# Kernel optimization log

Measured on AMD Instinct MI355X. Metric: run time of the kernel, lower is better.

Reference implementation:

```python
import jax, jax.numpy as jnp
import numpy as np

N_NODES = 100000  # size_u + size_v + size_w
N_MP = 3          # metapaths vv, uu, ww
N_EDGES = 1000000
D_IN = 64
D_OUT = 64


def setup_inputs() -> dict:
    key = jax.random.key(0)
    k1, k2, k3, k4 = jax.random.split(key, 4)
    x = jax.random.normal(k1, (N_NODES, D_IN), dtype=jnp.float32)
    # per-metapath GCNConv weight (glorot-ish scale)
    W = jax.random.normal(k2, (N_MP, D_IN, D_OUT), dtype=jnp.float32) * (1.0 / np.sqrt(D_IN))
    edge_index = jax.random.randint(k3, (N_MP, 2, N_EDGES), 0, N_NODES, dtype=jnp.int64)
    edge_weight = jax.random.uniform(k4, (N_MP, N_EDGES), dtype=jnp.float32)
    return {"x": x, "W": W, "edge_index": edge_index, "edge_weight": edge_weight}


def _gcn_conv(x, w_mat, row, col, ew, num_nodes):
    # gcn_norm without self-loops: deg[i] = sum of edge weights into i
    deg = jax.ops.segment_sum(ew, col, num_segments=num_nodes)
    dinv = jnp.where(deg > 0, jax.lax.rsqrt(jnp.where(deg > 0, deg, 1.0)), 0.0)
    norm = dinv[row] * ew * dinv[col]          # [E]
    h = x @ w_mat                               # [N, D_OUT]
    msg = h[row] * norm[:, None]                # [E, D_OUT] gather + scale
    return jax.ops.segment_sum(msg, col, num_segments=num_nodes)  # scatter-add


def reference(x, W, edge_index, edge_weight):
    num_nodes = x.shape[0]
    outs = []
    for i in range(N_MP):  # small fixed loop over structurally distinct encoders
        row = edge_index[i, 0]
        col = edge_index[i, 1]
        out = _gcn_conv(x, W[i], row, col, edge_weight[i], num_nodes)
        outs.append(jax.nn.relu(out))  # act=nn.ReLU
    return jnp.stack(outs)  # [3, N, D_OUT]; dropout omitted (eval mode)
```

## Files before the change

kernel.cpp:

```cpp
#include <hip/hip_runtime.h>
#include <hip/hip_fp16.h>

#define NNODES 100000
#define NMP 3
#define NEDGES 1000000
#define D 64
#define NTOT (NMP * NNODES)
#define BINW 1024
#define NBIN 293
#define CAPB 10944
#define T1 5632
#define RPT 11
#define OVCAP 131072

typedef __attribute__((ext_vector_type(8))) short bf16x8;
typedef __attribute__((ext_vector_type(4))) float floatx4;

__device__ __forceinline__ unsigned short f2bf(float f) {
    unsigned u = __float_as_uint(f);
    u = (u + 0x7FFFu + ((u >> 16) & 1u)) >> 16;
    return (unsigned short)u;
}
__device__ __forceinline__ __half2 u2h(unsigned u) {
    __half2 r;
    *reinterpret_cast<unsigned*>(&r) = u;
    return r;
}

__global__ __launch_bounds__(512) void split_kernel(const int* __restrict__ ei,
                                                    const float* __restrict__ ew,
                                                    int* __restrict__ gcur,
                                                    int* __restrict__ ovcur,
                                                    int* __restrict__ ovf,
                                                    uint2* __restrict__ A) {
    __shared__ uint2 stage[T1];
    __shared__ unsigned short sbin[T1];
    __shared__ int hist[NBIN], lbase[NBIN], gbase[NBIN], lcur[NBIN];
    __shared__ int sh[512];
    const int t = threadIdx.x;
    const int mp = blockIdx.y;
    const int e0 = blockIdx.x * T1;
    const int nrec = min(T1, NEDGES - e0);
    for (int i = t; i < NBIN; i += 512) hist[i] = 0;
    __syncthreads();
    unsigned key[RPT]; float w[RPT]; int bn[RPT];
#pragma unroll
    for (int i = 0; i < RPT; ++i) {
        int e = e0 + i * 512 + t;
        bn[i] = -1;
        if (e < NEDGES) {
            int r = ei[(mp * 2 + 0) * NEDGES + e];
            int c = ei[(mp * 2 + 1) * NEDGES + e];
            w[i] = ew[mp * NEDGES + e];
            int cflat = mp * NNODES + c;
            int rflat = mp * NNODES + r;
            int b = cflat >> 10;
            bn[i] = b;
            key[i] = ((unsigned)(cflat & 1023) << 19) | (unsigned)rflat;
            atomicAdd(&hist[b], 1);
        }
    }
    __syncthreads();
    int v = (t < NBIN) ? hist[t] : 0;
    sh[t] = v;
    __syncthreads();
    for (int d = 1; d < 512; d <<= 1) {
        int add = (t >= d) ? sh[t - d] : 0;
        __syncthreads();
        sh[t] += add;
        __syncthreads();
    }
    if (t < NBIN) {
        int ex = sh[t] - v;
        lbase[t] = ex;
        lcur[t] = ex;
        gbase[t] = v ? atomicAdd(&gcur[t], v) : 0;
    }
    __syncthreads();
#pragma unroll
    for (int i = 0; i < RPT; ++i) {
        if (bn[i] >= 0) {
            int s = atomicAdd(&lcur[bn[i]], 1);
            stage[s] = make_uint2(key[i], __float_as_uint(w[i]));
            sbin[s] = (unsigned short)bn[i];
        }
    }
    __syncthreads();
    for (int s = t; s < nrec; s += 512) {
        int b = sbin[s];
        uint2 rec = stage[s];
        int pos = gbase[b] + (s - lbase[b]);
        if (pos < CAPB) {
            A[(size_t)b * CAPB + pos] = rec;
        } else {
            int op = atomicAdd(ovcur, 1);
            if (op < OVCAP) {
                int cflat = (b << 10) | (int)(rec.x >> 19);
                ovf[3 * op] = cflat;
                ovf[3 * op + 1] = (int)(rec.x & 0x7FFFFu);
                ovf[3 * op + 2] = (int)rec.y;
            }
        }
    }
}

__global__ __launch_bounds__(256) void compact2_kernel(const int* __restrict__ gcur,
                                                       const uint2* __restrict__ A,
                                                       const int* __restrict__ ovcur,
                                                       const int* __restrict__ ovf,
                                                       uint2* __restrict__ C,
                                                       int2* __restrict__ nodeoff,
                                                       float* __restrict__ dinv) {
    const int bin = blockIdx.x;
    __shared__ int cnt[BINW];
    __shared__ float wsum[BINW];
    __shared__ int pos[BINW];
    __shared__ int sh[256];
    const int t = threadIdx.x;
    for (int i = t; i < BINW; i += 256) { cnt[i] = 0; wsum[i] = 0.0f; }
    __syncthreads();
    const int len = min(gcur[bin], CAPB);
    const uint2* Ab = A + (size_t)bin * CAPB;
    for (int p = t; p < len; p += 256) {
        uint2 rec = Ab[p];
        atomicAdd(&cnt[rec.x >> 19], 1);
        atomicAdd(&wsum[rec.x >> 19], __uint_as_float(rec.y));
    }
    const int ovn = min(*ovcur, OVCAP);
    for (int i = t; i < ovn; i += 256) {
        int cflat = ovf[3 * i];
        if ((cflat >> 10) == bin) {
            atomicAdd(&cnt[cflat & 1023], 1);
            atomicAdd(&wsum[cflat & 1023], __int_as_float(ovf[3 * i + 2]));
        }
    }
    __syncthreads();
    int c0 = cnt[4 * t], c1 = cnt[4 * t + 1], c2 = cnt[4 * t + 2], c3 = cnt[4 * t + 3];
    int vsum = c0 + c1 + c2 + c3;
    sh[t] = vsum;
    __syncthreads();
    for (int d = 1; d < 256; d <<= 1) {
        int add = (t >= d) ? sh[t - d] : 0;
        __syncthreads();
        sh[t] += add;
        __syncthreads();
    }
    const int base = bin * CAPB;
    const int lim = base + CAPB;
    int p0 = base + sh[t] - vsum;
    int p1 = p0 + c0, p2 = p1 + c1, p3 = p2 + c2;
    pos[4 * t] = p0; pos[4 * t + 1] = p1; pos[4 * t + 2] = p2; pos[4 * t + 3] = p3;
    int starts[4] = {p0, p1, p2, p3};
    int cs[4] = {c0, c1, c2, c3};
#pragma unroll
    for (int j = 0; j < 4; ++j) {
        int cl = 4 * t + j;
        int node = (bin << 10) + cl;
        if (node < NTOT) {
            nodeoff[node] = make_int2(starts[j], cs[j]);
            float dg = wsum[cl];
            dinv[node] = (dg > 0.0f) ? rsqrtf(dg) : 0.0f;
        }
    }
    __syncthreads();
    for (int p = t; p < len; p += 256) {
        uint2 rec = Ab[p];
        int s = atomicAdd(&pos[rec.x >> 19], 1);
        if (s < lim) C[s] = make_uint2(rec.x & 0x7FFFFu, rec.y);
    }
    for (int i = t; i < ovn; i += 256) {
        int cflat = ovf[3 * i];
        if ((cflat >> 10) == bin) {
            int s = atomicAdd(&pos[cflat & 1023], 1);
            if (s < lim) C[s] = make_uint2((unsigned)ovf[3 * i + 1], (unsigned)ovf[3 * i + 2]);
        }
    }
}

__global__ __launch_bounds__(256) void prep_w_kernel(const float* __restrict__ W,
                                                     unsigned short* __restrict__ wT) {
    int idx = blockIdx.x * 256 + threadIdx.x;
    if (idx >= NMP * D * D) return;
    int mp = idx >> 12, rem = idx & 4095;
    int k = rem >> 6, n = rem & 63;
    wT[(mp * D + n) * D + k] = f2bf(W[idx]);
}

__global__ __launch_bounds__(256) void gemm_kernel(const float* __restrict__ x,
                                                   const unsigned short* __restrict__ wT,
                                                   const float* __restrict__ dinv,
                                                   unsigned short* __restrict__ h) {
    const int wave = threadIdx.x >> 6;
    const int lane = threadIdx.x & 63;
    const int rowbase = (blockIdx.x * 4 + wave) * 16;
    if (rowbase >= NNODES) return;
    const int m = lane & 15;
    const int q = lane >> 4;
    const float4* xr = (const float4*)(x + (size_t)(rowbase + m) * D);
    bf16x8 a[2];
#pragma unroll
    for (int kc = 0; kc < 2; ++kc) {
        float4 x0 = xr[kc * 8 + q * 2];
        float4 x1 = xr[kc * 8 + q * 2 + 1];
        a[kc][0] = f2bf(x0.x); a[kc][1] = f2bf(x0.y);
        a[kc][2] = f2bf(x0.z); a[kc][3] = f2bf(x0.w);
        a[kc][4] = f2bf(x1.x); a[kc][5] = f2bf(x1.y);
        a[kc][6] = f2bf(x1.z); a[kc][7] = f2bf(x1.w);
    }
#pragma unroll
    for (int mp = 0; mp < NMP; ++mp) {
        float dv = dinv[mp * NNODES + rowbase + m];
#pragma unroll
        for (int nt = 0; nt < 4; ++nt) {
            const bf16x8* bp = (const bf16x8*)(wT + (size_t)(mp * D + nt * 16 + m) * D);
            bf16x8 b0 = bp[q];
            bf16x8 b1 = bp[4 + q];
            floatx4 acc = {0.f, 0.f, 0.f, 0.f};
            acc = __builtin_amdgcn_mfma_f32_16x16x32_bf16(b0, a[0], acc, 0, 0, 0);
            acc = __builtin_amdgcn_mfma_f32_16x16x32_bf16(b1, a[1], acc, 0, 0, 0);
            unsigned v0 = (unsigned)__half_as_ushort(__float2half(acc[0] * dv)) |
                          ((unsigned)__half_as_ushort(__float2half(acc[1] * dv)) << 16);
            unsigned v1 = (unsigned)__half_as_ushort(__float2half(acc[2] * dv)) |
                          ((unsigned)__half_as_ushort(__float2half(acc[3] * dv)) << 16);
            *(uint2*)(h + ((size_t)mp * NNODES + rowbase + m) * D + nt * 16 + q * 4) =
                make_uint2(v0, v1);
        }
    }
}

__global__ __launch_bounds__(256) void gather_kernel(const int2* __restrict__ nodeoff,
                                                     const uint2* __restrict__ dense,
                                                     const unsigned short* __restrict__ h,
                                                     const float* __restrict__ dinv,
                                                     float* __restrict__ out) {
    const int tid = threadIdx.x;
    const int wave = tid >> 6, lane = tid & 63;
    const int sub = lane >> 5;
    const int g = (lane >> 3) & 3;
    const int f = lane & 7;
    const int w = blockIdx.x * 8 + wave * 2 + sub;
    int2 off = nodeoff[w];
    const int start = off.x, end = off.x + off.y;
    const uint4* hp = (const uint4*)h;
    __half2 acc2[4];
    acc2[0] = __float2half2_rn(0.0f); acc2[1] = __float2half2_rn(0.0f);
    acc2[2] = __float2half2_rn(0.0f); acc2[3] = __float2half2_rn(0.0f);
    if (end > start) {
        const int last = end - 1;
        uint2 prA = dense[min(start + g, last)];
        uint2 prB = dense[min(start + 4 + g, last)];
        uint4 hvA = hp[(size_t)prA.x * 8 + f];
        for (int p = start; p < end; p += 4) {
            uint2 prC = dense[min(p + 8 + g, last)];
            uint4 hvB = hp[(size_t)prB.x * 8 + f];
            float wgt = (p + g < end) ? __uint_as_float(prA.y) : 0.0f;
            __half2 wp = __float2half2_rn(wgt);
            acc2[0] = __hfma2(u2h(hvA.x), wp, acc2[0]);
            acc2[1] = __hfma2(u2h(hvA.y), wp, acc2[1]);
            acc2[2] = __hfma2(u2h(hvA.z), wp, acc2[2]);
            acc2[3] = __hfma2(u2h(hvA.w), wp, acc2[3]);
            prA = prB; hvA = hvB; prB = prC;
        }
    }
    float acc[8];
    acc[0] = __low2float(acc2[0]); acc[1] = __high2float(acc2[0]);
    acc[2] = __low2float(acc2[1]); acc[3] = __high2float(acc2[1]);
    acc[4] = __low2float(acc2[2]); acc[5] = __high2float(acc2[2]);
    acc[6] = __low2float(acc2[3]); acc[7] = __high2float(acc2[3]);
#pragma unroll
    for (int j = 0; j < 8; ++j) {
        acc[j] += __shfl_xor(acc[j], 8);
        acc[j] += __shfl_xor(acc[j], 16);
    }
    float dv = dinv[w];
    if (g < 2) {
        float4 o = g ? make_float4(acc[4], acc[5], acc[6], acc[7])
                     : make_float4(acc[0], acc[1], acc[2], acc[3]);
        o.x = fmaxf(o.x * dv, 0.0f);
        o.y = fmaxf(o.y * dv, 0.0f);
        o.z = fmaxf(o.z * dv, 0.0f);
        o.w = fmaxf(o.w * dv, 0.0f);
        ((float4*)out)[(size_t)w * 16 + f * 2 + g] = o;
    }
}

extern "C" void kernel_launch(void* const* d_in, const int* in_sizes, int n_in,
                              void* d_out, int out_size, void* d_ws, size_t ws_size,
                              hipStream_t stream) {
    const float* x  = (const float*)d_in[0];
    const float* W  = (const float*)d_in[1];
    const int*   ei = (const int*)d_in[2];
    const float* ew = (const float*)d_in[3];
    float* out = (float*)d_out;

    char* ws = (char*)d_ws;
    uint2* A           = (uint2*)(ws + 0);
    unsigned short* h  = (unsigned short*)(ws + 0);
    uint2* C           = (uint2*)(ws + 38400000);
    int2*  nodeoff     = (int2*)(ws + 64052736);
    float* dinv        = (float*)(ws + 66452736);
    unsigned short* wT = (unsigned short*)(ws + 67652736);
    int*   gcur        = (int*)(ws + 67677312);
    int*   ovcur       = (int*)(ws + 67678484);
    int*   ovf         = (int*)(ws + 67678488);

    hipMemsetAsync(gcur, 0, 1176, stream);

    split_kernel<<<dim3((NEDGES + T1 - 1) / T1, NMP), 512, 0, stream>>>(ei, ew, gcur,
                                                                        ovcur, ovf, A);
    compact2_kernel<<<NBIN, 256, 0, stream>>>(gcur, A, ovcur, ovf, C, nodeoff, dinv);
    prep_w_kernel<<<(NMP * D * D + 255) / 256, 256, 0, stream>>>(W, wT);
    gemm_kernel<<<(NNODES / 16 + 3) / 4, 256, 0, stream>>>(x, wT, dinv, h);
    gather_kernel<<<NTOT / 8, 256, 0, stream>>>(nodeoff, C, h, dinv, out);
}
```

Measured before the change: 285.6 us.

## Use wave-shuffle block scans, widen compact blocks, one node per wave in gather

```diff
diff --git a/kernel.cpp b/kernel.cpp
--- a/kernel.cpp
+++ b/kernel.cpp
@@ -27,6 +27,31 @@
     return r;
 }
 
+__device__ __forceinline__ int block_excl_scan(int v, int t, int nthreads, int* wsums) {
+    const int lane = t & 63, wv = t >> 6;
+    int s = v;
+#pragma unroll
+    for (int d = 1; d < 64; d <<= 1) {
+        int u = __shfl_up(s, d);
+        if (lane >= d) s += u;
+    }
+    if (lane == 63) wsums[wv] = s;
+    __syncthreads();
+    if (wv == 0) {
+        const int nw = nthreads >> 6;
+        int ws = (lane < nw) ? wsums[lane] : 0;
+#pragma unroll
+        for (int d = 1; d < 8; d <<= 1) {
+            int u = __shfl_up(ws, d);
+            if (lane >= d) ws += u;
+        }
+        if (lane < nw) wsums[lane] = ws;
+    }
+    __syncthreads();
+    int wbase = wv ? wsums[wv - 1] : 0;
+    return wbase + s - v;
+}
+
 __global__ __launch_bounds__(512) void split_kernel(const int* __restrict__ ei,
                                                     const float* __restrict__ ew,
                                                     int* __restrict__ gcur,
@@ -36,7 +61,7 @@
     __shared__ uint2 stage[T1];
     __shared__ unsigned short sbin[T1];
     __shared__ int hist[NBIN], lbase[NBIN], gbase[NBIN], lcur[NBIN];
-    __shared__ int sh[512];
+    __shared__ int wsums[8];
     const int t = threadIdx.x;
     const int mp = blockIdx.y;
     const int e0 = blockIdx.x * T1;
@@ -62,16 +87,8 @@
     }
     __syncthreads();
     int v = (t < NBIN) ? hist[t] : 0;
-    sh[t] = v;
-    __syncthreads();
-    for (int d = 1; d < 512; d <<= 1) {
-        int add = (t >= d) ? sh[t - d] : 0;
-        __syncthreads();
-        sh[t] += add;
-        __syncthreads();
-    }
+    int ex = block_excl_scan(v, t, 512, wsums);
     if (t < NBIN) {
-        int ex = sh[t] - v;
         lbase[t] = ex;
         lcur[t] = ex;
         gbase[t] = v ? atomicAdd(&gcur[t], v) : 0;
@@ -104,7 +121,7 @@
     }
 }
 
-__global__ __launch_bounds__(256) void compact2_kernel(const int* __restrict__ gcur,
+__global__ __launch_bounds__(512) void compact2_kernel(const int* __restrict__ gcur,
                                                        const uint2* __restrict__ A,
                                                        const int* __restrict__ ovcur,
                                                        const int* __restrict__ ovf,
@@ -115,19 +132,19 @@
     __shared__ int cnt[BINW];
     __shared__ float wsum[BINW];
     __shared__ int pos[BINW];
-    __shared__ int sh[256];
+    __shared__ int wsums[8];
     const int t = threadIdx.x;
-    for (int i = t; i < BINW; i += 256) { cnt[i] = 0; wsum[i] = 0.0f; }
+    for (int i = t; i < BINW; i += 512) { cnt[i] = 0; wsum[i] = 0.0f; }
     __syncthreads();
     const int len = min(gcur[bin], CAPB);
     const uint2* Ab = A + (size_t)bin * CAPB;
-    for (int p = t; p < len; p += 256) {
+    for (int p = t; p < len; p += 512) {
         uint2 rec = Ab[p];
         atomicAdd(&cnt[rec.x >> 19], 1);
         atomicAdd(&wsum[rec.x >> 19], __uint_as_float(rec.y));
     }
     const int ovn = min(*ovcur, OVCAP);
-    for (int i = t; i < ovn; i += 256) {
+    for (int i = t; i < ovn; i += 512) {
         int cflat = ovf[3 * i];
         if ((cflat >> 10) == bin) {
             atomicAdd(&cnt[cflat & 1023], 1);
@@ -135,26 +152,18 @@
         }
     }
     __syncthreads();
-    int c0 = cnt[4 * t], c1 = cnt[4 * t + 1], c2 = cnt[4 * t + 2], c3 = cnt[4 * t + 3];
-    int vsum = c0 + c1 + c2 + c3;
-    sh[t] = vsum;
-    __syncthreads();
-    for (int d = 1; d < 256; d <<= 1) {
-        int add = (t >= d) ? sh[t - d] : 0;
-        __syncthreads();
-        sh[t] += add;
-        __syncthreads();
-    }
+    int c0 = cnt[2 * t], c1 = cnt[2 * t + 1];
+    int ex = block_excl_scan(c0 + c1, t, 512, wsums);
     const int base = bin * CAPB;
     const int lim = base + CAPB;
-    int p0 = base + sh[t] - vsum;
-    int p1 = p0 + c0, p2 = p1 + c1, p3 = p2 + c2;
-    pos[4 * t] = p0; pos[4 * t + 1] = p1; pos[4 * t + 2] = p2; pos[4 * t + 3] = p3;
-    int starts[4] = {p0, p1, p2, p3};
-    int cs[4] = {c0, c1, c2, c3};
-#pragma unroll
-    for (int j = 0; j < 4; ++j) {
-        int cl = 4 * t + j;
+    int p0 = base + ex;
+    int p1 = p0 + c0;
+    pos[2 * t] = p0; pos[2 * t + 1] = p1;
+    int starts[2] = {p0, p1};
+    int cs[2] = {c0, c1};
+#pragma unroll
+    for (int j = 0; j < 2; ++j) {
+        int cl = 2 * t + j;
         int node = (bin << 10) + cl;
         if (node < NTOT) {
             nodeoff[node] = make_int2(starts[j], cs[j]);
@@ -163,12 +172,12 @@
         }
     }
     __syncthreads();
-    for (int p = t; p < len; p += 256) {
+    for (int p = t; p < len; p += 512) {
         uint2 rec = Ab[p];
         int s = atomicAdd(&pos[rec.x >> 19], 1);
         if (s < lim) C[s] = make_uint2(rec.x & 0x7FFFFu, rec.y);
     }
-    for (int i = t; i < ovn; i += 256) {
+    for (int i = t; i < ovn; i += 512) {
         int cflat = ovf[3 * i];
         if ((cflat >> 10) == bin) {
             int s = atomicAdd(&pos[cflat & 1023], 1);
@@ -235,10 +244,9 @@
                                                      float* __restrict__ out) {
     const int tid = threadIdx.x;
     const int wave = tid >> 6, lane = tid & 63;
-    const int sub = lane >> 5;
-    const int g = (lane >> 3) & 3;
+    const int g = lane >> 3;
     const int f = lane & 7;
-    const int w = blockIdx.x * 8 + wave * 2 + sub;
+    const int w = blockIdx.x * 4 + wave;
     int2 off = nodeoff[w];
     const int start = off.x, end = off.x + off.y;
     const uint4* hp = (const uint4*)h;
@@ -248,10 +256,10 @@
     if (end > start) {
         const int last = end - 1;
         uint2 prA = dense[min(start + g, last)];
-        uint2 prB = dense[min(start + 4 + g, last)];
+        uint2 prB = dense[min(start + 8 + g, last)];
         uint4 hvA = hp[(size_t)prA.x * 8 + f];
-        for (int p = start; p < end; p += 4) {
-            uint2 prC = dense[min(p + 8 + g, last)];
+        for (int p = start; p < end; p += 8) {
+            uint2 prC = dense[min(p + 16 + g, last)];
             uint4 hvB = hp[(size_t)prB.x * 8 + f];
             float wgt = (p + g < end) ? __uint_as_float(prA.y) : 0.0f;
             __half2 wp = __float2half2_rn(wgt);
@@ -271,6 +279,7 @@
     for (int j = 0; j < 8; ++j) {
         acc[j] += __shfl_xor(acc[j], 8);
         acc[j] += __shfl_xor(acc[j], 16);
+        acc[j] += __shfl_xor(acc[j], 32);
     }
     float dv = dinv[w];
     if (g < 2) {
@@ -308,8 +317,8 @@
 
     split_kernel<<<dim3((NEDGES + T1 - 1) / T1, NMP), 512, 0, stream>>>(ei, ew, gcur,
                                                                         ovcur, ovf, A);
-    compact2_kernel<<<NBIN, 256, 0, stream>>>(gcur, A, ovcur, ovf, C, nodeoff, dinv);
+    compact2_kernel<<<NBIN, 512, 0, stream>>>(gcur, A, ovcur, ovf, C, nodeoff, dinv);
     prep_w_kernel<<<(NMP * D * D + 255) / 256, 256, 0, stream>>>(W, wT);
     gemm_kernel<<<(NNODES / 16 + 3) / 4, 256, 0, stream>>>(x, wT, dinv, h);
-    gather_kernel<<<NTOT / 8, 256, 0, stream>>>(nodeoff, C, h, dinv, out);
-}
+    gather_kernel<<<NTOT / 4, 256, 0, stream>>>(nodeoff, C, h, dinv, out);
+}
```

Result: slower. 313.3 us (+9.7%).
